# Kernel optimization log

Hardware: AMD Instinct MI355X
Metric: run time of the kernel (lower is better)

## Reference

```python
import jax, jax.numpy as jnp
import numpy as np


def _unfold3x3(x):
    # Matches torch F.unfold(kernel=(3,3), padding=1): output (B, C*9, H*W)
    # with feature layout (c, kh, kw) -- channel-major, kernel-position minor.
    B, C, H, W = x.shape
    xp = jnp.pad(x, ((0, 0), (0, 0), (1, 1), (1, 1)))
    patches = jnp.stack(
        [xp[:, :, i:i + H, j:j + W] for i in range(3) for j in range(3)],
        axis=2,
    )  # (B, C, 9, H, W)
    return patches.reshape(B, C * 9, H * W)


def setup_inputs() -> dict:
    key = jax.random.key(0)
    x = jax.random.normal(key, (4, 64, 64, 64), dtype=jnp.float32)
    return {"x": x}


def reference(x):
    B, C, H, W = x.shape
    HW = H * W
    xu = _unfold3x3(x)  # (B, C*9, HW)
    # torch F.normalize(dim=2): L2-normalize each (b, feature) row over spatial dim
    norm = jnp.maximum(jnp.linalg.norm(xu, axis=2, keepdims=True), 1e-12)
    xu = xu / norm
    # dense correlation over all positions: (B, HW, HW)
    R = jnp.einsum('bdn,bdm->bnm', xu, xu)
    _, idx = jax.lax.top_k(R, 3)  # idx: (B, HW, 3)
    # gather the top-3 neighbor patch columns; fixed k=3 loop (structural, not data dim)
    stacks = []
    for k in range(3):
        idx_k = idx[:, :, k][:, None, :]                    # (B, 1, HW)
        g = jnp.take_along_axis(xu, idx_k, axis=2)          # (B, C*9, HW)
        # torch: permute(0,2,1).reshape(B, HW, -1, C) -> (B, HW, 9, C)
        stacks.append(jnp.transpose(g, (0, 2, 1)).reshape(B, HW, 9, C))
    K = jnp.concatenate(stacks, axis=2)                     # (B, HW, 27, C)
    Q = jnp.transpose(x.reshape(B, C, HW), (0, 2, 1))       # (B, HW, C)
    scores = jnp.einsum('bnc,bnkc->bnk', Q, K) / jnp.sqrt(jnp.float32(C))
    w = jax.nn.softmax(scores, axis=2)                      # (B, HW, 27)
    return jnp.einsum('bnk,bnkc->bnc', w, K)                # (B, HW, C)
```

## Files before the change

### kernel.cpp

```cpp
#include <hip/hip_runtime.h>
#include <cstdint>

typedef short short8 __attribute__((ext_vector_type(8)));
typedef float f32x16 __attribute__((ext_vector_type(16)));

#define NB 4
#define NN 4096
#define ND 576
#define BIGI 0x7FFFFFFF
#define NSLICE 8

#define INVN_OFF 9437184
#define CANDV_OFF 9439488
#define CANDI_OFF 9832704

#define MFMA __builtin_amdgcn_mfma_f32_32x32x16_bf16

__device__ __forceinline__ unsigned short f2bf(float f) {
    unsigned u = __float_as_uint(f);
    u += 0x7FFFu + ((u >> 16) & 1u);
    return (unsigned short)(u >> 16);
}

__device__ __forceinline__ void gload_lds16(const void* g, void* l) {
    __builtin_amdgcn_global_load_lds(
        (const __attribute__((address_space(1))) void*)g,
        (__attribute__((address_space(3))) void*)l, 16, 0, 0);
}

__device__ __forceinline__ void insert_cmp(float v, int m,
    float& v0, int& i0, float& v1, int& i1, float& v2, int& i2) {
    bool beat2 = (v > v2) || (v == v2 && m < i2);
    if (beat2) {
        bool beat1 = (v > v1) || (v == v1 && m < i1);
        if (beat1) {
            v2 = v1; i2 = i1;
            bool beat0 = (v > v0) || (v == v0 && m < i0);
            if (beat0) { v1 = v0; i1 = i0; v0 = v; i0 = m; }
            else       { v1 = v;  i1 = m; }
        } else { v2 = v; i2 = m; }
    }
}

__global__ __launch_bounds__(64) void norm_kernel(const float* __restrict__ x,
                                                  float* __restrict__ ws) {
    const int bc = blockIdx.x;
    const int lane = threadIdx.x;
    const float* xp = x + ((size_t)bc << 12);
    float colsum = 0.f, v0 = 0.f, v63 = 0.f;
    for (int h = 0; h < 64; ++h) {
        const float val = xp[(h << 6) + lane];
        const float sq = val * val;
        colsum += sq;
        if (h == 0)  v0 = sq;
        if (h == 63) v63 = sq;
    }
    float total = colsum, row0 = v0, row63 = v63;
    #pragma unroll
    for (int o = 32; o > 0; o >>= 1) {
        total += __shfl_xor(total, o);
        row0  += __shfl_xor(row0, o);
        row63 += __shfl_xor(row63, o);
    }
    const float col0  = __shfl(colsum, 0);
    const float col63 = __shfl(colsum, 63);
    const float c00 = __shfl(v0, 0),  c0e = __shfl(v0, 63);
    const float ce0 = __shfl(v63, 0), cee = __shfl(v63, 63);
    if (lane < 9) {
        const int dh = lane / 3 - 1, dw = lane % 3 - 1;
        float S = total;
        if (dh == 1)  S -= row0;
        if (dh == -1) S -= row63;
        if (dw == 1)  S -= col0;
        if (dw == -1) S -= col63;
        if (dh == 1  && dw == 1)  S += c00;
        if (dh == 1  && dw == -1) S += c0e;
        if (dh == -1 && dw == 1)  S += ce0;
        if (dh == -1 && dw == -1) S += cee;
        float nrm = fmaxf(sqrtf(S), 1e-12f);
        ws[INVN_OFF + bc * 9 + lane] = 1.0f / nrm;
    }
}

__global__ __launch_bounds__(256) void mat_kernel(const float* __restrict__ x,
                                                  float* __restrict__ ws) {
    const int bi = blockIdx.x;
    const int b = bi / 576;
    const int rem = bi - b * 576;
    const int nt = rem / 18;
    const int kc = rem - nt * 18;
    unsigned short* AH = (unsigned short*)ws;
    unsigned short* AL = AH + 9437184;
    const float* invn = ws + INVN_OFF + b * 576;
    const int tid = threadIdx.x;
    #pragma unroll
    for (int hf2 = 0; hf2 < 2; ++hf2) {
        const int g = tid + hf2 * 256;
        const int row = g >> 2, cp = g & 3;
        const int c = cp ^ ((row >> 1) & 3);
        const int k0 = c * 8;
        const int n = nt * 128 + row;
        const int h = n >> 6, wc = n & 63;
        union { unsigned short us[8]; float4 f4; } uh, ul;
        #pragma unroll
        for (int j = 0; j < 8; ++j) {
            const int d = kc * 32 + k0 + j;
            const int ch = d / 9;
            const int p = d - ch * 9;
            const int r = h + p / 3 - 1, s2 = wc + p % 3 - 1;
            float val = 0.f;
            if ((unsigned)r < 64u && (unsigned)s2 < 64u)
                val = x[((size_t)(b * 64 + ch) << 12) + (r << 6) + s2];
            val *= invn[d];
            const unsigned short hb = f2bf(val);
            const float hfv = __uint_as_float(((unsigned)hb) << 16);
            const unsigned short lb = f2bf(val - hfv);
            uh.us[j] = hb; ul.us[j] = lb;
        }
        ((float4*)AH)[(size_t)bi * 512 + g] = uh.f4;
        ((float4*)AL)[(size_t)bi * 512 + g] = ul.f4;
    }
}

__device__ __forceinline__ short8 ldfrag(const short* p) {
    union { short8 s8; float4 f4; } u;
    u.f4 = *(const float4*)p;
    return u.s8;
}

__global__ void __launch_bounds__(256, 2) gram_kernel(float* ws) {
    __shared__ short sm[24576];
    const int bx = blockIdx.x;
    const int b = bx >> 8;
    const int nt = (bx >> 3) & 31;
    const int s = bx & 7;
    const int tid = threadIdx.x;
    const int w = tid >> 6, lane = tid & 63;
    const int l31 = lane & 31, kh2 = lane >> 5;

    const unsigned short* AH = (const unsigned short*)ws;
    const unsigned short* AL = AH + 9437184;

    const int AnH = 0, AnL = 4096, AmH = 8192, AmL = 16384;
    const int nRegBase = (b * 32 + nt) * 18;

    float t0v[4], t1v[4], t2v[4];
    int   t0i[4], t1i[4], t2i[4];
    #pragma unroll
    for (int i = 0; i < 4; ++i) {
        t0v[i] = t1v[i] = t2v[i] = -INFINITY;
        t0i[i] = t1i[i] = t2i[i] = BIGI;
    }

    int aoff[2][2];
    int boff[4][2];
    #pragma unroll
    for (int mi = 0; mi < 2; ++mi)
        #pragma unroll
        for (int h = 0; h < 2; ++h) {
            const int row = w * 64 + mi * 32 + l31;
            const int rl = row & 127, rt = row >> 7;
            const int c = kh2 + 2 * h;
            aoff[mi][h] = rt * 4096 + rl * 32 + (c ^ ((rl >> 1) & 3)) * 8;
        }
    #pragma unroll
    for (int ni = 0; ni < 4; ++ni)
        #pragma unroll
        for (int h = 0; h < 2; ++h) {
            const int row = ni * 32 + l31;
            const int c = kh2 + 2 * h;
            boff[ni][h] = row * 32 + (c ^ ((row >> 1) & 3)) * 8;
        }

    for (int mt = 0; mt < 2; ++mt) {
        const int p = s * 2 + mt;
        const int mReg0 = (b * 32 + 2 * p) * 18;
        const int mReg1 = mReg0 + 18;

        f32x16 acc[2][4];
        #pragma unroll
        for (int mi = 0; mi < 2; ++mi)
            #pragma unroll
            for (int ni = 0; ni < 4; ++ni)
                #pragma unroll
                for (int e = 0; e < 16; ++e) acc[mi][ni][e] = 0.f;

        for (int kc = 0; kc < 18; ++kc) {
            __syncthreads();
            {
                const int lo0 = (w * 2) * 512, lo1 = (w * 2 + 1) * 512;
                const int go0 = lo0 + lane * 8, go1 = lo1 + lane * 8;
                const unsigned short* gAnH = AH + (size_t)(nRegBase + kc) * 4096;
                const unsigned short* gAnL = AL + (size_t)(nRegBase + kc) * 4096;
                const unsigned short* gM0H = AH + (size_t)(mReg0 + kc) * 4096;
                const unsigned short* gM1H = AH + (size_t)(mReg1 + kc) * 4096;
                const unsigned short* gM0L = AL + (size_t)(mReg0 + kc) * 4096;
                const unsigned short* gM1L = AL + (size_t)(mReg1 + kc) * 4096;
                gload_lds16(gAnH + go0, sm + AnH + lo0);
                gload_lds16(gAnH + go1, sm + AnH + lo1);
                gload_lds16(gAnL + go0, sm + AnL + lo0);
                gload_lds16(gAnL + go1, sm + AnL + lo1);
                gload_lds16(gM0H + go0, sm + AmH + lo0);
                gload_lds16(gM0H + go1, sm + AmH + lo1);
                gload_lds16(gM1H + go0, sm + AmH + 4096 + lo0);
                gload_lds16(gM1H + go1, sm + AmH + 4096 + lo1);
                gload_lds16(gM0L + go0, sm + AmL + lo0);
                gload_lds16(gM0L + go1, sm + AmL + lo1);
                gload_lds16(gM1L + go0, sm + AmL + 4096 + lo0);
                gload_lds16(gM1L + go1, sm + AmL + 4096 + lo1);
            }
            __syncthreads();
            #pragma unroll
            for (int h = 0; h < 2; ++h) {
                short8 amh[2], aml[2];
                #pragma unroll
                for (int mi = 0; mi < 2; ++mi) {
                    amh[mi] = ldfrag(sm + AmH + aoff[mi][h]);
                    aml[mi] = ldfrag(sm + AmL + aoff[mi][h]);
                }
                #pragma unroll
                for (int ni = 0; ni < 4; ++ni) {
                    const short8 bh = ldfrag(sm + AnH + boff[ni][h]);
                    const short8 bl = ldfrag(sm + AnL + boff[ni][h]);
                    #pragma unroll
                    for (int mi = 0; mi < 2; ++mi) {
                        acc[mi][ni] = MFMA(amh[mi], bh, acc[mi][ni], 0, 0, 0);
                        acc[mi][ni] = MFMA(amh[mi], bl, acc[mi][ni], 0, 0, 0);
                        acc[mi][ni] = MFMA(aml[mi], bh, acc[mi][ni], 0, 0, 0);
                    }
                }
            }
        }
        const int mbase = p * 256 + w * 64 + kh2 * 4;
        #pragma unroll
        for (int ni = 0; ni < 4; ++ni)
            #pragma unroll
            for (int mi = 0; mi < 2; ++mi)
                #pragma unroll
                for (int v = 0; v < 16; ++v) {
                    const int m = mbase + mi * 32 + (v & 3) + 8 * (v >> 2);
                    insert_cmp(acc[mi][ni][v], m,
                               t0v[ni], t0i[ni], t1v[ni], t1i[ni], t2v[ni], t2i[ni]);
                }
    }

    #pragma unroll
    for (int ni = 0; ni < 4; ++ni) {
        const float pv0 = __shfl_xor(t0v[ni], 32);
        const float pv1 = __shfl_xor(t1v[ni], 32);
        const float pv2 = __shfl_xor(t2v[ni], 32);
        const int pi0 = __shfl_xor(t0i[ni], 32);
        const int pi1 = __shfl_xor(t1i[ni], 32);
        const int pi2 = __shfl_xor(t2i[ni], 32);
        insert_cmp(pv0, pi0, t0v[ni], t0i[ni], t1v[ni], t1i[ni], t2v[ni], t2i[ni]);
        insert_cmp(pv1, pi1, t0v[ni], t0i[ni], t1v[ni], t1i[ni], t2v[ni], t2i[ni]);
        insert_cmp(pv2, pi2, t0v[ni], t0i[ni], t1v[ni], t1i[ni], t2v[ni], t2i[ni]);
    }
    __syncthreads();
    float* cv = (float*)sm;
    int*   ci = (int*)sm + 1536;
    if (kh2 == 0) {
        #pragma unroll
        for (int ni = 0; ni < 4; ++ni) {
            const int base = ((w * 4 + ni) * 32 + l31) * 3;
            cv[base] = t0v[ni]; cv[base + 1] = t1v[ni]; cv[base + 2] = t2v[ni];
            ci[base] = t0i[ni]; ci[base + 1] = t1i[ni]; ci[base + 2] = t2i[ni];
        }
    }
    __syncthreads();
    if (tid < 128) {
        const int ni = tid >> 5, l = tid & 31;
        float v0 = -INFINITY, v1 = -INFINITY, v2 = -INFINITY;
        int i0 = BIGI, i1 = BIGI, i2 = BIGI;
        #pragma unroll
        for (int w2 = 0; w2 < 4; ++w2) {
            const int base = ((w2 * 4 + ni) * 32 + l) * 3;
            #pragma unroll
            for (int j = 0; j < 3; ++j)
                insert_cmp(cv[base + j], ci[base + j], v0, i0, v1, i1, v2, i2);
        }
        const int n_local = ni * 32 + l;
        const size_t o = ((size_t)(b * NSLICE + s) * NN + nt * 128 + n_local) * 3;
        ws[CANDV_OFF + o] = v0; ws[CANDV_OFF + o + 1] = v1; ws[CANDV_OFF + o + 2] = v2;
        unsigned short* wi = (unsigned short*)(ws + CANDI_OFF);
        wi[o] = (unsigned short)i0; wi[o + 1] = (unsigned short)i1; wi[o + 2] = (unsigned short)i2;
    }
}

__global__ __launch_bounds__(256) void attn_kernel(const float* __restrict__ x,
                                                   const float* __restrict__ ws,
                                                   float* __restrict__ out) {
    const int wid = threadIdx.x >> 6;
    const int lane = threadIdx.x & 63;
    const int gw = blockIdx.x * 4 + wid;
    const int b = gw >> 12;
    const int n = gw & 4095;

    float v0 = -INFINITY, v1 = -INFINITY, v2 = -INFINITY;
    int i0 = BIGI, i1 = BIGI, i2 = BIGI;
    const unsigned short* wi = (const unsigned short*)(ws + CANDI_OFF);
    #pragma unroll
    for (int s = 0; s < NSLICE; ++s) {
        const size_t o = ((size_t)(b * NSLICE + s) * NN + n) * 3;
        #pragma unroll
        for (int j = 0; j < 3; ++j)
            insert_cmp(ws[CANDV_OFF + o + j], (int)wi[o + j], v0, i0, v1, i1, v2, i2);
    }
    const int idx3[3] = {i0, i1, i2};

    int cc[9], dhh[9], dww[9];
    float inr[9];
    #pragma unroll
    for (int a = 0; a < 9; ++a) {
        const int d = a * 64 + lane;
        const int c = d / 9;
        const int p = d - c * 9;
        cc[a] = c; dhh[a] = p / 3 - 1; dww[a] = p - (p / 3) * 3 - 1;
        inr[a] = ws[INVN_OFF + b * ND + d];
    }
    const float q = x[((size_t)(b * 64 + lane) << 12) + n];

    float rv[27], sc[27];
    #pragma unroll
    for (int k = 0; k < 3; ++k) {
        const int m = idx3[k];
        const int hm = m >> 6, wm = m & 63;
        #pragma unroll
        for (int a = 0; a < 9; ++a) {
            const int r = hm + dhh[a], s2 = wm + dww[a];
            float val = 0.f;
            if ((unsigned)r < 64u && (unsigned)s2 < 64u)
                val = x[((size_t)(b * 64 + cc[a]) << 12) + (r << 6) + s2];
            const float rr = val * inr[a];
            rv[k * 9 + a] = rr;
            float t = q * rr;
            #pragma unroll
            for (int o2 = 32; o2 > 0; o2 >>= 1) t += __shfl_xor(t, o2);
            sc[k * 9 + a] = t * 0.125f;
        }
    }
    float mx = -INFINITY;
    #pragma unroll
    for (int u = 0; u < 27; ++u) mx = fmaxf(mx, sc[u]);
    float sum = 0.f;
    #pragma unroll
    for (int u = 0; u < 27; ++u) { const float e = expf(sc[u] - mx); sc[u] = e; sum += e; }
    const float inv = 1.0f / sum;
    float o = 0.f;
    #pragma unroll
    for (int u = 0; u < 27; ++u) o += sc[u] * rv[u];
    out[((size_t)gw << 6) + lane] = o * inv;
}

extern "C" void kernel_launch(void* const* d_in, const int* in_sizes, int n_in,
                              void* d_out, int out_size, void* d_ws, size_t ws_size,
                              hipStream_t stream) {
    (void)in_sizes; (void)n_in; (void)out_size; (void)ws_size;
    const float* x = (const float*)d_in[0];
    float* ws = (float*)d_ws;
    float* out = (float*)d_out;

    hipLaunchKernelGGL(norm_kernel, dim3(NB * 64), dim3(64), 0, stream, x, ws);
    hipLaunchKernelGGL(mat_kernel, dim3(2304), dim3(256), 0, stream, x, ws);
    hipLaunchKernelGGL(gram_kernel, dim3(1024), dim3(256), 0, stream, ws);
    hipLaunchKernelGGL(attn_kernel, dim3(4096), dim3(256), 0, stream, x, ws, out);
}
```

Measured before the change: 717.0 us.

## Exploit Gram matrix symmetry to compute only upper-triangular tile pairs

Gram blocks now enumerate only tile pairs (nt, mp) with mp at or above nt/2, using 272 blocks per batch instead of 256 blocks that each covered two m-tiles. Off-diagonal tiles also do a column-wise top-3 reduction with shuffles and write candidates for the transposed rows into per-row variable-length candidate lists. This roughly halves the MFMA work of the dense correlation. In exchange it adds a transposed reduction, scattered candidate writes, and longer per-row merge lists in the attention kernel.

```diff
diff --git a/kernel.cpp b/kernel.cpp
--- a/kernel.cpp
+++ b/kernel.cpp
@@ -8,11 +8,11 @@
 #define NN 4096
 #define ND 576
 #define BIGI 0x7FFFFFFF
-#define NSLICE 8
 
 #define INVN_OFF 9437184
 #define CANDV_OFF 9439488
-#define CANDI_OFF 9832704
+#define LPB 96256
+#define CANDI_OFF 10594560
 
 #define MFMA __builtin_amdgcn_mfma_f32_32x32x16_bf16
 
@@ -26,6 +26,11 @@
     __builtin_amdgcn_global_load_lds(
         (const __attribute__((address_space(1))) void*)g,
         (__attribute__((address_space(3))) void*)l, 16, 0, 0);
+}
+
+__device__ __forceinline__ int list_base(int b, int n) {
+    const int K = n >> 8;
+    return b * LPB + 16 * n + 128 * K * (K - 1) + (n & 255) * K;
 }
 
 __device__ __forceinline__ void insert_cmp(float v, int m,
@@ -130,10 +135,12 @@
 
 __global__ void __launch_bounds__(256, 2) gram_kernel(float* ws) {
     __shared__ short sm[24576];
-    const int bx = blockIdx.x;
-    const int b = bx >> 8;
-    const int nt = (bx >> 3) & 31;
-    const int s = bx & 7;
+    const int t = blockIdx.x;
+    const int b = t / 272;
+    const int r = t - b * 272;
+    int mp = 0;
+    while ((mp + 1) * (mp + 2) <= r) ++mp;
+    const int nt = r - mp * (mp + 1);
     const int tid = threadIdx.x;
     const int w = tid >> 6, lane = tid & 63;
     const int l31 = lane & 31, kh2 = lane >> 5;
@@ -143,14 +150,8 @@
 
     const int AnH = 0, AnL = 4096, AmH = 8192, AmL = 16384;
     const int nRegBase = (b * 32 + nt) * 18;
-
-    float t0v[4], t1v[4], t2v[4];
-    int   t0i[4], t1i[4], t2i[4];
-    #pragma unroll
-    for (int i = 0; i < 4; ++i) {
-        t0v[i] = t1v[i] = t2v[i] = -INFINITY;
-        t0i[i] = t1i[i] = t2i[i] = BIGI;
-    }
+    const int mReg0 = (b * 32 + 2 * mp) * 18;
+    const int mReg1 = mReg0 + 18;
 
     int aoff[2][2];
     int boff[4][2];
@@ -172,76 +173,111 @@
             boff[ni][h] = row * 32 + (c ^ ((row >> 1) & 3)) * 8;
         }
 
-    for (int mt = 0; mt < 2; ++mt) {
-        const int p = s * 2 + mt;
-        const int mReg0 = (b * 32 + 2 * p) * 18;
-        const int mReg1 = mReg0 + 18;
-
-        f32x16 acc[2][4];
-        #pragma unroll
-        for (int mi = 0; mi < 2; ++mi)
-            #pragma unroll
-            for (int ni = 0; ni < 4; ++ni)
-                #pragma unroll
-                for (int e = 0; e < 16; ++e) acc[mi][ni][e] = 0.f;
-
-        for (int kc = 0; kc < 18; ++kc) {
-            __syncthreads();
-            {
-                const int lo0 = (w * 2) * 512, lo1 = (w * 2 + 1) * 512;
-                const int go0 = lo0 + lane * 8, go1 = lo1 + lane * 8;
-                const unsigned short* gAnH = AH + (size_t)(nRegBase + kc) * 4096;
-                const unsigned short* gAnL = AL + (size_t)(nRegBase + kc) * 4096;
-                const unsigned short* gM0H = AH + (size_t)(mReg0 + kc) * 4096;
-                const unsigned short* gM1H = AH + (size_t)(mReg1 + kc) * 4096;
-                const unsigned short* gM0L = AL + (size_t)(mReg0 + kc) * 4096;
-                const unsigned short* gM1L = AL + (size_t)(mReg1 + kc) * 4096;
-                gload_lds16(gAnH + go0, sm + AnH + lo0);
-                gload_lds16(gAnH + go1, sm + AnH + lo1);
-                gload_lds16(gAnL + go0, sm + AnL + lo0);
-                gload_lds16(gAnL + go1, sm + AnL + lo1);
-                gload_lds16(gM0H + go0, sm + AmH + lo0);
-                gload_lds16(gM0H + go1, sm + AmH + lo1);
-                gload_lds16(gM1H + go0, sm + AmH + 4096 + lo0);
-                gload_lds16(gM1H + go1, sm + AmH + 4096 + lo1);
-                gload_lds16(gM0L + go0, sm + AmL + lo0);
-                gload_lds16(gM0L + go1, sm + AmL + lo1);
-                gload_lds16(gM1L + go0, sm + AmL + 4096 + lo0);
-                gload_lds16(gM1L + go1, sm + AmL + 4096 + lo1);
+    float t0v[4], t1v[4], t2v[4];
+    int   t0i[4], t1i[4], t2i[4];
+    #pragma unroll
+    for (int i = 0; i < 4; ++i) {
+        t0v[i] = t1v[i] = t2v[i] = -INFINITY;
+        t0i[i] = t1i[i] = t2i[i] = BIGI;
+    }
+
+    f32x16 acc[2][4];
+    #pragma unroll
+    for (int mi = 0; mi < 2; ++mi)
+        #pragma unroll
+        for (int ni = 0; ni < 4; ++ni)
+            #pragma unroll
+            for (int e = 0; e < 16; ++e) acc[mi][ni][e] = 0.f;
+
+    for (int kc = 0; kc < 18; ++kc) {
+        __syncthreads();
+        {
+            const int lo0 = (w * 2) * 512, lo1 = (w * 2 + 1) * 512;
+            const int go0 = lo0 + lane * 8, go1 = lo1 + lane * 8;
+            const unsigned short* gAnH = AH + (size_t)(nRegBase + kc) * 4096;
+            const unsigned short* gAnL = AL + (size_t)(nRegBase + kc) * 4096;
+            const unsigned short* gM0H = AH + (size_t)(mReg0 + kc) * 4096;
+            const unsigned short* gM1H = AH + (size_t)(mReg1 + kc) * 4096;
+            const unsigned short* gM0L = AL + (size_t)(mReg0 + kc) * 4096;
+            const unsigned short* gM1L = AL + (size_t)(mReg1 + kc) * 4096;
+            gload_lds16(gAnH + go0, sm + AnH + lo0);
+            gload_lds16(gAnH + go1, sm + AnH + lo1);
+            gload_lds16(gAnL + go0, sm + AnL + lo0);
+            gload_lds16(gAnL + go1, sm + AnL + lo1);
+            gload_lds16(gM0H + go0, sm + AmH + lo0);
+            gload_lds16(gM0H + go1, sm + AmH + lo1);
+            gload_lds16(gM1H + go0, sm + AmH + 4096 + lo0);
+            gload_lds16(gM1H + go1, sm + AmH + 4096 + lo1);
+            gload_lds16(gM0L + go0, sm + AmL + lo0);
+            gload_lds16(gM0L + go1, sm + AmL + lo1);
+            gload_lds16(gM1L + go0, sm + AmL + 4096 + lo0);
+            gload_lds16(gM1L + go1, sm + AmL + 4096 + lo1);
+        }
+        __syncthreads();
+        #pragma unroll
+        for (int h = 0; h < 2; ++h) {
+            short8 amh[2], aml[2];
+            #pragma unroll
+            for (int mi = 0; mi < 2; ++mi) {
+                amh[mi] = ldfrag(sm + AmH + aoff[mi][h]);
+                aml[mi] = ldfrag(sm + AmL + aoff[mi][h]);
             }
-            __syncthreads();
-            #pragma unroll
-            for (int h = 0; h < 2; ++h) {
-                short8 amh[2], aml[2];
+            #pragma unroll
+            for (int ni = 0; ni < 4; ++ni) {
+                const short8 bh = ldfrag(sm + AnH + boff[ni][h]);
+                const short8 bl = ldfrag(sm + AnL + boff[ni][h]);
                 #pragma unroll
                 for (int mi = 0; mi < 2; ++mi) {
-                    amh[mi] = ldfrag(sm + AmH + aoff[mi][h]);
-                    aml[mi] = ldfrag(sm + AmL + aoff[mi][h]);
-                }
-                #pragma unroll
-                for (int ni = 0; ni < 4; ++ni) {
-                    const short8 bh = ldfrag(sm + AnH + boff[ni][h]);
-                    const short8 bl = ldfrag(sm + AnL + boff[ni][h]);
-                    #pragma unroll
-                    for (int mi = 0; mi < 2; ++mi) {
-                        acc[mi][ni] = MFMA(amh[mi], bh, acc[mi][ni], 0, 0, 0);
-                        acc[mi][ni] = MFMA(amh[mi], bl, acc[mi][ni], 0, 0, 0);
-                        acc[mi][ni] = MFMA(aml[mi], bh, acc[mi][ni], 0, 0, 0);
-                    }
+                    acc[mi][ni] = MFMA(amh[mi], bh, acc[mi][ni], 0, 0, 0);
+                    acc[mi][ni] = MFMA(amh[mi], bl, acc[mi][ni], 0, 0, 0);
+                    acc[mi][ni] = MFMA(aml[mi], bh, acc[mi][ni], 0, 0, 0);
                 }
             }
         }
-        const int mbase = p * 256 + w * 64 + kh2 * 4;
-        #pragma unroll
-        for (int ni = 0; ni < 4; ++ni)
-            #pragma unroll
-            for (int mi = 0; mi < 2; ++mi)
+    }
+
+    unsigned short* wsi = (unsigned short*)(ws + CANDI_OFF);
+
+    const int mbase = mp * 256 + w * 64 + kh2 * 4;
+    #pragma unroll
+    for (int ni = 0; ni < 4; ++ni)
+        #pragma unroll
+        for (int mi = 0; mi < 2; ++mi)
+            #pragma unroll
+            for (int v = 0; v < 16; ++v) {
+                const int m = mbase + mi * 32 + (v & 3) + 8 * (v >> 2);
+                insert_cmp(acc[mi][ni][v], m,
+                           t0v[ni], t0i[ni], t1v[ni], t1i[ni], t2v[ni], t2i[ni]);
+            }
+
+    if (mp > (nt >> 1)) {
+        #pragma unroll
+        for (int mi = 0; mi < 2; ++mi) {
+            #pragma unroll
+            for (int v = 0; v < 16; ++v) {
+                float q0 = -INFINITY, q1 = -INFINITY, q2 = -INFINITY;
+                int j0 = BIGI, j1 = BIGI, j2 = BIGI;
                 #pragma unroll
-                for (int v = 0; v < 16; ++v) {
+                for (int ni = 0; ni < 4; ++ni)
+                    insert_cmp(acc[mi][ni][v], nt * 128 + ni * 32 + l31,
+                               q0, j0, q1, j1, q2, j2);
+                #pragma unroll
+                for (int o = 1; o < 32; o <<= 1) {
+                    const float p0 = __shfl_xor(q0, o), p1 = __shfl_xor(q1, o), p2 = __shfl_xor(q2, o);
+                    const int a0 = __shfl_xor(j0, o), a1 = __shfl_xor(j1, o), a2 = __shfl_xor(j2, o);
+                    insert_cmp(p0, a0, q0, j0, q1, j1, q2, j2);
+                    insert_cmp(p1, a1, q0, j0, q1, j1, q2, j2);
+                    insert_cmp(p2, a2, q0, j0, q1, j1, q2, j2);
+                }
+                if (l31 == 0) {
                     const int m = mbase + mi * 32 + (v & 3) + 8 * (v >> 2);
-                    insert_cmp(acc[mi][ni][v], m,
-                               t0v[ni], t0i[ni], t1v[ni], t1i[ni], t2v[ni], t2i[ni]);
+                    const size_t lb = (size_t)list_base(b, m) + (16 - mp + nt);
+                    const size_t off = lb * 3;
+                    ws[CANDV_OFF + off] = q0; ws[CANDV_OFF + off + 1] = q1; ws[CANDV_OFF + off + 2] = q2;
+                    wsi[off] = (unsigned short)j0; wsi[off + 1] = (unsigned short)j1; wsi[off + 2] = (unsigned short)j2;
                 }
+            }
+        }
     }
 
     #pragma unroll
@@ -279,11 +315,11 @@
             for (int j = 0; j < 3; ++j)
                 insert_cmp(cv[base + j], ci[base + j], v0, i0, v1, i1, v2, i2);
         }
-        const int n_local = ni * 32 + l;
-        const size_t o = ((size_t)(b * NSLICE + s) * NN + nt * 128 + n_local) * 3;
+        const int n_glob = nt * 128 + ni * 32 + l;
+        const size_t lb = (size_t)list_base(b, n_glob) + (mp - (nt >> 1));
+        const size_t o = lb * 3;
         ws[CANDV_OFF + o] = v0; ws[CANDV_OFF + o + 1] = v1; ws[CANDV_OFF + o + 2] = v2;
-        unsigned short* wi = (unsigned short*)(ws + CANDI_OFF);
-        wi[o] = (unsigned short)i0; wi[o + 1] = (unsigned short)i1; wi[o + 2] = (unsigned short)i2;
+        wsi[o] = (unsigned short)i0; wsi[o + 1] = (unsigned short)i1; wsi[o + 2] = (unsigned short)i2;
     }
 }
 
@@ -299,12 +335,13 @@
     float v0 = -INFINITY, v1 = -INFINITY, v2 = -INFINITY;
     int i0 = BIGI, i1 = BIGI, i2 = BIGI;
     const unsigned short* wi = (const unsigned short*)(ws + CANDI_OFF);
-    #pragma unroll
-    for (int s = 0; s < NSLICE; ++s) {
-        const size_t o = ((size_t)(b * NSLICE + s) * NN + n) * 3;
-        #pragma unroll
-        for (int j = 0; j < 3; ++j)
-            insert_cmp(ws[CANDV_OFF + o + j], (int)wi[o + j], v0, i0, v1, i1, v2, i2);
+    const int cnt = 16 + (n >> 8);
+    const size_t base = (size_t)list_base(b, n);
+    for (int j = 0; j < cnt; ++j) {
+        const size_t o = (base + j) * 3;
+        #pragma unroll
+        for (int u = 0; u < 3; ++u)
+            insert_cmp(ws[CANDV_OFF + o + u], (int)wi[o + u], v0, i0, v1, i1, v2, i2);
     }
     const int idx3[3] = {i0, i1, i2};
 
@@ -362,6 +399,6 @@
 
     hipLaunchKernelGGL(norm_kernel, dim3(NB * 64), dim3(64), 0, stream, x, ws);
     hipLaunchKernelGGL(mat_kernel, dim3(2304), dim3(256), 0, stream, x, ws);
-    hipLaunchKernelGGL(gram_kernel, dim3(1024), dim3(256), 0, stream, ws);
+    hipLaunchKernelGGL(gram_kernel, dim3(1088), dim3(256), 0, stream, ws);
     hipLaunchKernelGGL(attn_kernel, dim3(4096), dim3(256), 0, stream, x, ws, out);
 }
```

Result: slower. 1.203 ms (+67.8%).

## Retile gram kernel to 256x256 blocks with double-buffered async LDS loads

Applied to the files above, without the earlier changes.

The gram kernel now runs 512 threads per block, each computing a 256x256 output tile. A block-swizzled mapping (I,J) picks the tiles for better L2 locality. Global-to-LDS loads are double buffered with explicit vmcnt waits and raw s_barrier, so the next k-chunk's load overlaps the MFMAs. This replaces the old 128x256 tile done as two sequential m-passes with full syncthreads. Top-3 candidates are now written per 256-column slice, so NSLICE doubles to 16, which means more candidate storage and more merge work in attn_kernel. LDS use rises to 128KB per block, which may limit occupancy.

```diff
diff --git a/kernel.cpp b/kernel.cpp
--- a/kernel.cpp
+++ b/kernel.cpp
@@ -8,11 +8,11 @@
 #define NN 4096
 #define ND 576
 #define BIGI 0x7FFFFFFF
-#define NSLICE 8
+#define NSLICE 16
 
 #define INVN_OFF 9437184
 #define CANDV_OFF 9439488
-#define CANDI_OFF 9832704
+#define CANDI_OFF 10225920
 
 #define MFMA __builtin_amdgcn_mfma_f32_32x32x16_bf16
 
@@ -128,21 +128,97 @@
     return u.s8;
 }
 
-__global__ void __launch_bounds__(256, 2) gram_kernel(float* ws) {
-    __shared__ short sm[24576];
+__global__ void __launch_bounds__(512, 2) gram_kernel(float* ws) {
+    __shared__ short sm[65536];
     const int bx = blockIdx.x;
     const int b = bx >> 8;
-    const int nt = (bx >> 3) & 31;
-    const int s = bx & 7;
+    const int t = bx & 255;
+    const int x = t & 7, g = t >> 3;
+    const int I = (x >> 1) * 4 + (g >> 3);
+    const int J = (x & 1) * 8 + (g & 7);
     const int tid = threadIdx.x;
     const int w = tid >> 6, lane = tid & 63;
+    const int wn = w >> 2, wm = w & 3;
     const int l31 = lane & 31, kh2 = lane >> 5;
 
     const unsigned short* AH = (const unsigned short*)ws;
     const unsigned short* AL = AH + 9437184;
 
-    const int AnH = 0, AnL = 4096, AmH = 8192, AmL = 16384;
-    const int nRegBase = (b * 32 + nt) * 18;
+    const unsigned short* gplane = (((w >> 1) & 1) == 0) ? AH : AL;
+    const int gtile = (w < 4) ? (2 * I + (w & 1)) : (2 * J + (w & 1));
+    const unsigned short* gbase = gplane + (size_t)((b * 32 + gtile) * 18) * 4096;
+    const int ldsReg = w * 4096;
+
+    int aoff[2][2];
+    int boff[4][2];
+    #pragma unroll
+    for (int mi = 0; mi < 2; ++mi)
+        #pragma unroll
+        for (int h = 0; h < 2; ++h) {
+            const int row = (wm & 1) * 64 + mi * 32 + l31;
+            const int c = kh2 + 2 * h;
+            aoff[mi][h] = (wm >> 1) * 4096 + row * 32 + (c ^ ((row >> 1) & 3)) * 8;
+        }
+    #pragma unroll
+    for (int ni = 0; ni < 4; ++ni)
+        #pragma unroll
+        for (int h = 0; h < 2; ++h) {
+            const int row = ni * 32 + l31;
+            const int c = kh2 + 2 * h;
+            boff[ni][h] = wn * 4096 + row * 32 + (c ^ ((row >> 1) & 3)) * 8;
+        }
+
+    f32x16 acc[2][4];
+    #pragma unroll
+    for (int mi = 0; mi < 2; ++mi)
+        #pragma unroll
+        for (int ni = 0; ni < 4; ++ni)
+            #pragma unroll
+            for (int e = 0; e < 16; ++e) acc[mi][ni][e] = 0.f;
+
+    {
+        const unsigned short* gs = gbase;
+        short* dst = sm + ldsReg;
+        #pragma unroll
+        for (int i = 0; i < 8; ++i)
+            gload_lds16(gs + i * 512 + lane * 8, dst + i * 512 + lane * 8);
+    }
+
+    for (int kc = 0; kc < 18; ++kc) {
+        if (kc < 17) {
+            const unsigned short* gs = gbase + (size_t)(kc + 1) * 4096;
+            short* dst = sm + ((kc + 1) & 1) * 32768 + ldsReg;
+            #pragma unroll
+            for (int i = 0; i < 8; ++i)
+                gload_lds16(gs + i * 512 + lane * 8, dst + i * 512 + lane * 8);
+            asm volatile("s_waitcnt vmcnt(8)" ::: "memory");
+        } else {
+            asm volatile("s_waitcnt vmcnt(0)" ::: "memory");
+        }
+        asm volatile("s_barrier" ::: "memory");
+        const short* base = sm + (kc & 1) * 32768;
+        #pragma unroll
+        for (int h = 0; h < 2; ++h) {
+            short8 amh[2], aml[2];
+            #pragma unroll
+            for (int mi = 0; mi < 2; ++mi) {
+                amh[mi] = ldfrag(base + 16384 + aoff[mi][h]);
+                aml[mi] = ldfrag(base + 24576 + aoff[mi][h]);
+            }
+            #pragma unroll
+            for (int ni = 0; ni < 4; ++ni) {
+                const short8 bh = ldfrag(base + boff[ni][h]);
+                const short8 bl = ldfrag(base + 8192 + boff[ni][h]);
+                #pragma unroll
+                for (int mi = 0; mi < 2; ++mi) {
+                    acc[mi][ni] = MFMA(amh[mi], bh, acc[mi][ni], 0, 0, 0);
+                    acc[mi][ni] = MFMA(amh[mi], bl, acc[mi][ni], 0, 0, 0);
+                    acc[mi][ni] = MFMA(aml[mi], bh, acc[mi][ni], 0, 0, 0);
+                }
+            }
+        }
+        asm volatile("s_barrier" ::: "memory");
+    }
 
     float t0v[4], t1v[4], t2v[4];
     int   t0i[4], t1i[4], t2i[4];
@@ -151,98 +227,17 @@
         t0v[i] = t1v[i] = t2v[i] = -INFINITY;
         t0i[i] = t1i[i] = t2i[i] = BIGI;
     }
-
-    int aoff[2][2];
-    int boff[4][2];
-    #pragma unroll
-    for (int mi = 0; mi < 2; ++mi)
-        #pragma unroll
-        for (int h = 0; h < 2; ++h) {
-            const int row = w * 64 + mi * 32 + l31;
-            const int rl = row & 127, rt = row >> 7;
-            const int c = kh2 + 2 * h;
-            aoff[mi][h] = rt * 4096 + rl * 32 + (c ^ ((rl >> 1) & 3)) * 8;
-        }
+    const int mbase = J * 256 + wm * 64 + kh2 * 4;
     #pragma unroll
     for (int ni = 0; ni < 4; ++ni)
         #pragma unroll
-        for (int h = 0; h < 2; ++h) {
-            const int row = ni * 32 + l31;
-            const int c = kh2 + 2 * h;
-            boff[ni][h] = row * 32 + (c ^ ((row >> 1) & 3)) * 8;
-        }
-
-    for (int mt = 0; mt < 2; ++mt) {
-        const int p = s * 2 + mt;
-        const int mReg0 = (b * 32 + 2 * p) * 18;
-        const int mReg1 = mReg0 + 18;
-
-        f32x16 acc[2][4];
-        #pragma unroll
         for (int mi = 0; mi < 2; ++mi)
             #pragma unroll
-            for (int ni = 0; ni < 4; ++ni)
-                #pragma unroll
-                for (int e = 0; e < 16; ++e) acc[mi][ni][e] = 0.f;
-
-        for (int kc = 0; kc < 18; ++kc) {
-            __syncthreads();
-            {
-                const int lo0 = (w * 2) * 512, lo1 = (w * 2 + 1) * 512;
-                const int go0 = lo0 + lane * 8, go1 = lo1 + lane * 8;
-                const unsigned short* gAnH = AH + (size_t)(nRegBase + kc) * 4096;
-                const unsigned short* gAnL = AL + (size_t)(nRegBase + kc) * 4096;
-                const unsigned short* gM0H = AH + (size_t)(mReg0 + kc) * 4096;
-                const unsigned short* gM1H = AH + (size_t)(mReg1 + kc) * 4096;
-                const unsigned short* gM0L = AL + (size_t)(mReg0 + kc) * 4096;
-                const unsigned short* gM1L = AL + (size_t)(mReg1 + kc) * 4096;
-                gload_lds16(gAnH + go0, sm + AnH + lo0);
-                gload_lds16(gAnH + go1, sm + AnH + lo1);
-                gload_lds16(gAnL + go0, sm + AnL + lo0);
-                gload_lds16(gAnL + go1, sm + AnL + lo1);
-                gload_lds16(gM0H + go0, sm + AmH + lo0);
-                gload_lds16(gM0H + go1, sm + AmH + lo1);
-                gload_lds16(gM1H + go0, sm + AmH + 4096 + lo0);
-                gload_lds16(gM1H + go1, sm + AmH + 4096 + lo1);
-                gload_lds16(gM0L + go0, sm + AmL + lo0);
-                gload_lds16(gM0L + go1, sm + AmL + lo1);
-                gload_lds16(gM1L + go0, sm + AmL + 4096 + lo0);
-                gload_lds16(gM1L + go1, sm + AmL + 4096 + lo1);
+            for (int v = 0; v < 16; ++v) {
+                const int m = mbase + mi * 32 + (v & 3) + 8 * (v >> 2);
+                insert_cmp(acc[mi][ni][v], m,
+                           t0v[ni], t0i[ni], t1v[ni], t1i[ni], t2v[ni], t2i[ni]);
             }
-            __syncthreads();
-            #pragma unroll
-            for (int h = 0; h < 2; ++h) {
-                short8 amh[2], aml[2];
-                #pragma unroll
-                for (int mi = 0; mi < 2; ++mi) {
-                    amh[mi] = ldfrag(sm + AmH + aoff[mi][h]);
-                    aml[mi] = ldfrag(sm + AmL + aoff[mi][h]);
-                }
-                #pragma unroll
-                for (int ni = 0; ni < 4; ++ni) {
-                    const short8 bh = ldfrag(sm + AnH + boff[ni][h]);
-                    const short8 bl = ldfrag(sm + AnL + boff[ni][h]);
-                    #pragma unroll
-                    for (int mi = 0; mi < 2; ++mi) {
-                        acc[mi][ni] = MFMA(amh[mi], bh, acc[mi][ni], 0, 0, 0);
-                        acc[mi][ni] = MFMA(amh[mi], bl, acc[mi][ni], 0, 0, 0);
-                        acc[mi][ni] = MFMA(aml[mi], bh, acc[mi][ni], 0, 0, 0);
-                    }
-                }
-            }
-        }
-        const int mbase = p * 256 + w * 64 + kh2 * 4;
-        #pragma unroll
-        for (int ni = 0; ni < 4; ++ni)
-            #pragma unroll
-            for (int mi = 0; mi < 2; ++mi)
-                #pragma unroll
-                for (int v = 0; v < 16; ++v) {
-                    const int m = mbase + mi * 32 + (v & 3) + 8 * (v >> 2);
-                    insert_cmp(acc[mi][ni][v], m,
-                               t0v[ni], t0i[ni], t1v[ni], t1i[ni], t2v[ni], t2i[ni]);
-                }
-    }
 
     #pragma unroll
     for (int ni = 0; ni < 4; ++ni) {
@@ -258,29 +253,30 @@
     }
     __syncthreads();
     float* cv = (float*)sm;
-    int*   ci = (int*)sm + 1536;
+    int*   ci = (int*)sm + 3072;
     if (kh2 == 0) {
         #pragma unroll
         for (int ni = 0; ni < 4; ++ni) {
-            const int base = ((w * 4 + ni) * 32 + l31) * 3;
-            cv[base] = t0v[ni]; cv[base + 1] = t1v[ni]; cv[base + 2] = t2v[ni];
-            ci[base] = t0i[ni]; ci[base + 1] = t1i[ni]; ci[base + 2] = t2i[ni];
+            const int base2 = ((w * 4 + ni) * 32 + l31) * 3;
+            cv[base2] = t0v[ni]; cv[base2 + 1] = t1v[ni]; cv[base2 + 2] = t2v[ni];
+            ci[base2] = t0i[ni]; ci[base2 + 1] = t1i[ni]; ci[base2 + 2] = t2i[ni];
         }
     }
     __syncthreads();
-    if (tid < 128) {
-        const int ni = tid >> 5, l = tid & 31;
+    if (tid < 256) {
+        const int wnr = tid >> 7, rl = tid & 127;
+        const int ni = rl >> 5, l = rl & 31;
         float v0 = -INFINITY, v1 = -INFINITY, v2 = -INFINITY;
         int i0 = BIGI, i1 = BIGI, i2 = BIGI;
         #pragma unroll
-        for (int w2 = 0; w2 < 4; ++w2) {
-            const int base = ((w2 * 4 + ni) * 32 + l) * 3;
+        for (int wm2 = 0; wm2 < 4; ++wm2) {
+            const int base2 = (((wnr * 4 + wm2) * 4 + ni) * 32 + l) * 3;
             #pragma unroll
             for (int j = 0; j < 3; ++j)
-                insert_cmp(cv[base + j], ci[base + j], v0, i0, v1, i1, v2, i2);
-        }
-        const int n_local = ni * 32 + l;
-        const size_t o = ((size_t)(b * NSLICE + s) * NN + nt * 128 + n_local) * 3;
+                insert_cmp(cv[base2 + j], ci[base2 + j], v0, i0, v1, i1, v2, i2);
+        }
+        const int n_glob = (2 * I + wnr) * 128 + ni * 32 + l;
+        const size_t o = ((size_t)(b * NSLICE + J) * NN + n_glob) * 3;
         ws[CANDV_OFF + o] = v0; ws[CANDV_OFF + o + 1] = v1; ws[CANDV_OFF + o + 2] = v2;
         unsigned short* wi = (unsigned short*)(ws + CANDI_OFF);
         wi[o] = (unsigned short)i0; wi[o + 1] = (unsigned short)i1; wi[o + 2] = (unsigned short)i2;
@@ -299,7 +295,6 @@
     float v0 = -INFINITY, v1 = -INFINITY, v2 = -INFINITY;
     int i0 = BIGI, i1 = BIGI, i2 = BIGI;
     const unsigned short* wi = (const unsigned short*)(ws + CANDI_OFF);
-    #pragma unroll
     for (int s = 0; s < NSLICE; ++s) {
         const size_t o = ((size_t)(b * NSLICE + s) * NN + n) * 3;
         #pragma unroll
@@ -362,6 +357,6 @@
 
     hipLaunchKernelGGL(norm_kernel, dim3(NB * 64), dim3(64), 0, stream, x, ws);
     hipLaunchKernelGGL(mat_kernel, dim3(2304), dim3(256), 0, stream, x, ws);
-    hipLaunchKernelGGL(gram_kernel, dim3(1024), dim3(256), 0, stream, ws);
+    hipLaunchKernelGGL(gram_kernel, dim3(1024), dim3(512), 0, stream, ws);
     hipLaunchKernelGGL(attn_kernel, dim3(4096), dim3(256), 0, stream, x, ws, out);
 }
```

After: 811.6 us. 13.2% more time.
